# Kernel optimization log

Measured on AMD Instinct MI355X. Metric: run time of the kernel, lower is better.

## Reference

```python
import jax, jax.numpy as jnp
import numpy as np
import math

D_MODEL = 512
NHEAD = 8
HEAD_DIM = D_MODEL // NHEAD
MAX_REL = 128
B, T, S = 4, 2048, 2048


def setup_inputs() -> dict:
    key = jax.random.key(0)
    ks = jax.random.split(key, 16)
    sc = 1.0 / math.sqrt(D_MODEL)
    inp = {
        "query": jax.random.normal(ks[0], (B, T, D_MODEL), jnp.float32),
        "key": jax.random.normal(ks[1], (B, S, D_MODEL), jnp.float32),
        "value": jax.random.normal(ks[2], (B, S, D_MODEL), jnp.float32),
        "Wq": jax.random.normal(ks[3], (D_MODEL, D_MODEL), jnp.float32) * sc,
        "bq": jnp.zeros((D_MODEL,), jnp.float32),
        "Wk": jax.random.normal(ks[4], (D_MODEL, D_MODEL), jnp.float32) * sc,
        "bk": jnp.zeros((D_MODEL,), jnp.float32),
        "Wv": jax.random.normal(ks[5], (D_MODEL, D_MODEL), jnp.float32) * sc,
        "bv": jnp.zeros((D_MODEL,), jnp.float32),
        "Wo": jax.random.normal(ks[6], (D_MODEL, D_MODEL), jnp.float32) * sc,
        "bo": jnp.zeros((D_MODEL,), jnp.float32),
        "rel_emb": jax.random.normal(ks[7], (2 * MAX_REL + 1, NHEAD), jnp.float32) * 0.02,
    }
    return inp


def reference(query, key, value, Wq, bq, Wk, bk, Wv, bv, Wo, bo, rel_emb):
    # linear projections (torch Linear: x @ W.T + b), split heads -> [B,H,T,Dh]
    def proj(x, W, b, L):
        return (x @ W.T + b).reshape(B, L, NHEAD, HEAD_DIM).transpose(0, 2, 1, 3)

    q = proj(query, Wq, bq, T)
    k = proj(key, Wk, bk, S)
    v = proj(value, Wv, bv, S)

    scores = jnp.einsum("bhtd,bhsd->bhts", q, k) / math.sqrt(HEAD_DIM)

    # relative position bias lookup: rel[t,s] = clamp(t-s) + max_rel -> [H,T,S]
    rel = jnp.arange(T)[:, None] - jnp.arange(S)[None, :]
    rel = jnp.clip(rel, -MAX_REL, MAX_REL) + MAX_REL
    bias = rel_emb[rel].transpose(2, 0, 1)  # [H,T,S]
    scores = scores + bias[None]

    w = jax.nn.softmax(scores, axis=-1)  # dropout p used in eval mode -> identity
    out = jnp.einsum("bhts,bhsd->bhtd", w, v)
    out = out.transpose(0, 2, 1, 3).reshape(B, T, D_MODEL)
    return out @ Wo.T + bo
```

## Files before the change

kernel.cpp:

```cpp
#include <hip/hip_runtime.h>

typedef __attribute__((ext_vector_type(4))) float f32x4;
typedef __attribute__((ext_vector_type(16))) float f32x16;
typedef __attribute__((ext_vector_type(4))) unsigned short u16x4;
typedef __attribute__((ext_vector_type(8))) unsigned short u16x8;
typedef __attribute__((ext_vector_type(4))) unsigned int u32x4;
typedef __attribute__((ext_vector_type(8))) __bf16 bf16x8;

#define SZX_E ((size_t)4 * 2048 * 512)
#define SZW_E ((size_t)512 * 512)

__device__ __forceinline__ unsigned short f2bf(float f) {
  unsigned int u = __builtin_bit_cast(unsigned int, f);
  u += 0x7fffu + ((u >> 16) & 1u);
  return (unsigned short)(u >> 16);
}

__device__ __forceinline__ bf16x8 ld_bf8(const unsigned short* p) {
  return __builtin_bit_cast(bf16x8, *(const u16x8*)p);
}

__device__ __forceinline__ f32x4 mfma16(bf16x8 a, bf16x8 b, f32x4 c) {
  return __builtin_amdgcn_mfma_f32_16x16x32_bf16(a, b, c, 0, 0, 0);
}

__device__ __forceinline__ f32x16 mfma32(bf16x8 a, bf16x8 b, f32x16 c) {
  return __builtin_amdgcn_mfma_f32_32x32x16_bf16(a, b, c, 0, 0, 0);
}

__device__ __forceinline__ unsigned int cvt_pk_bf16(float lo, float hi) {
  unsigned int r;
  asm("v_cvt_pk_bf16_f32 %0, %1, %2" : "=v"(r) : "v"(lo), "v"(hi));
  return r;
}

__device__ __forceinline__ void plane32_swap(unsigned int& a, unsigned int& b) {
  asm("v_permlane32_swap_b32 %0, %1" : "+v"(a), "+v"(b));
}

__device__ __forceinline__ float exp2_fast(float x) {
  float r;
  asm("v_exp_f32 %0, %1" : "=v"(r) : "v"(x));
  return r;
}

__device__ __forceinline__ void gload16(const void* g, void* l) {
  __builtin_amdgcn_global_load_lds(
      (const __attribute__((address_space(1))) unsigned int*)g,
      (__attribute__((address_space(3))) unsigned int*)l, 16, 0, 0);
}

__global__ __launch_bounds__(256) void cvt_all(const float* __restrict__ q_,
                                               const float* __restrict__ k_,
                                               const float* __restrict__ v_,
                                               const float* __restrict__ wq_,
                                               const float* __restrict__ wk_,
                                               const float* __restrict__ wv_,
                                               const float* __restrict__ wo_,
                                               unsigned short* __restrict__ out) {
  const int bq = blockIdx.x;
  const float* src;
  size_t segbase, li;
  if (bq < 12288) {
    const int s = bq >> 12;
    src = (s == 0) ? q_ : (s == 1) ? k_ : v_;
    li = (size_t)(bq & 4095) * 256 + threadIdx.x;
    segbase = (size_t)s * 4194304;
  } else {
    const int s = (bq - 12288) >> 8;
    src = (s == 0) ? wq_ : (s == 1) ? wk_ : (s == 2) ? wv_ : wo_;
    li = (size_t)((bq - 12288) & 255) * 256 + threadIdx.x;
    segbase = 12582912 + (size_t)s * 262144;
  }
  const f32x4 v = *(const f32x4*)(src + li * 4);
  u16x4 r;
  r[0] = f2bf(v[0]); r[1] = f2bf(v[1]); r[2] = f2bf(v[2]); r[3] = f2bf(v[3]);
  *(u16x4*)(out + segbase + li * 4) = r;
}

__global__ __launch_bounds__(256) void gemm_qkv(const unsigned short* __restrict__ base,
                                                const float* __restrict__ bq,
                                                const float* __restrict__ bk,
                                                const float* __restrict__ bv,
                                                unsigned short* __restrict__ outb) {
  __shared__ unsigned short Asb[2][4096];
  __shared__ unsigned short Bsb[2][4096];
  const int z = blockIdx.z;
  const unsigned short* A = base + (size_t)z * SZX_E;
  const unsigned short* Bw = base + 3 * SZX_E + (size_t)z * SZW_E;
  const float* bias = (z == 0) ? bq : (z == 1) ? bk : bv;

  const int tid = threadIdx.x;
  const int l = tid & 63;
  const int w = tid >> 6;
  const int g = l >> 4;
  const int lr = l & 15;
  const int mB = blockIdx.y * 128;
  const int nB = blockIdx.x * 128;
  const int m0 = (w >> 1) * 64;
  const int n0 = (w & 1) * 64;
  const int ubase = tid & ~63;

  auto stage = [&](int bufi, int kk) {
#pragma unroll
    for (int i = 0; i < 2; i++) {
      const int idx = i * 256 + tid;
      const int ub = i * 256 + ubase;
      const int r = idx >> 2, c = idx & 3;
      gload16((const char*)A + ((size_t)(mB + r) * 512 + kk + c * 8) * 2,
              (char*)&Asb[bufi][0] + ub * 16);
      gload16((const char*)Bw + ((size_t)(nB + r) * 512 + kk + c * 8) * 2,
              (char*)&Bsb[bufi][0] + ub * 16);
    }
  };

  f32x4 acc[4][4];
#pragma unroll
  for (int i = 0; i < 4; i++)
#pragma unroll
    for (int j = 0; j < 4; j++) acc[i][j] = f32x4{0.f, 0.f, 0.f, 0.f};

  stage(0, 0);
  __syncthreads();
  int buf = 0;

  for (int ks = 0; ks < 16; ++ks) {
    if (ks < 15) stage(buf ^ 1, (ks + 1) * 32);
    bf16x8 af[4], bfr[4];
#pragma unroll
    for (int t = 0; t < 4; t++) {
      af[t] = ld_bf8(&Asb[buf][(m0 + t * 16 + lr) * 32 + g * 8]);
      bfr[t] = ld_bf8(&Bsb[buf][(n0 + t * 16 + lr) * 32 + g * 8]);
    }
#pragma unroll
    for (int i = 0; i < 4; i++)
#pragma unroll
      for (int j = 0; j < 4; j++)
        acc[i][j] = mfma16(af[i], bfr[j], acc[i][j]);
    __syncthreads();
    buf ^= 1;
  }

  unsigned short* outz = outb + (size_t)z * SZX_E;
#pragma unroll
  for (int j = 0; j < 4; j++) {
    const int n = nB + n0 + j * 16 + lr;
    const float bn = bias[n];
#pragma unroll
    for (int i = 0; i < 4; i++) {
#pragma unroll
      for (int r = 0; r < 4; r++) {
        const int m = mB + m0 + i * 16 + g * 4 + r;
        const float v = acc[i][j][r] + bn;
        if (z < 2) {
          outz[(size_t)m * 512 + n] = f2bf(v);
        } else {
          const int bb = m >> 11, s = m & 2047;
          const int hh = n >> 6, d = n & 63;
          outz[((size_t)((bb * 8 + hh) * 64 + d) << 11) + s] = f2bf(v);
        }
      }
    }
  }
}

__global__ __launch_bounds__(256) void gemm_o(const unsigned short* __restrict__ A,
                                              const unsigned short* __restrict__ Bw,
                                              const float* __restrict__ bias,
                                              float* __restrict__ Cout) {
  __shared__ unsigned short Asb[2][4096];
  __shared__ unsigned short Bsb[2][4096];
  const int tid = threadIdx.x;
  const int l = tid & 63;
  const int w = tid >> 6;
  const int g = l >> 4;
  const int lr = l & 15;
  const int mB = blockIdx.y * 128;
  const int nB = blockIdx.x * 128;
  const int m0 = (w >> 1) * 64;
  const int n0 = (w & 1) * 64;
  const int ubase = tid & ~63;

  auto stage = [&](int bufi, int kk) {
#pragma unroll
    for (int i = 0; i < 2; i++) {
      const int idx = i * 256 + tid;
      const int ub = i * 256 + ubase;
      const int r = idx >> 2, c = idx & 3;
      gload16((const char*)A + ((size_t)(mB + r) * 512 + kk + c * 8) * 2,
              (char*)&Asb[bufi][0] + ub * 16);
      gload16((const char*)Bw + ((size_t)(nB + r) * 512 + kk + c * 8) * 2,
              (char*)&Bsb[bufi][0] + ub * 16);
    }
  };

  f32x4 acc[4][4];
#pragma unroll
  for (int i = 0; i < 4; i++)
#pragma unroll
    for (int j = 0; j < 4; j++) acc[i][j] = f32x4{0.f, 0.f, 0.f, 0.f};

  stage(0, 0);
  __syncthreads();
  int buf = 0;

  for (int ks = 0; ks < 16; ++ks) {
    if (ks < 15) stage(buf ^ 1, (ks + 1) * 32);
    bf16x8 af[4], bfr[4];
#pragma unroll
    for (int t = 0; t < 4; t++) {
      af[t] = ld_bf8(&Asb[buf][(m0 + t * 16 + lr) * 32 + g * 8]);
      bfr[t] = ld_bf8(&Bsb[buf][(n0 + t * 16 + lr) * 32 + g * 8]);
    }
#pragma unroll
    for (int i = 0; i < 4; i++)
#pragma unroll
      for (int j = 0; j < 4; j++)
        acc[i][j] = mfma16(af[i], bfr[j], acc[i][j]);
    __syncthreads();
    buf ^= 1;
  }

#pragma unroll
  for (int j = 0; j < 4; j++) {
    const int n = nB + n0 + j * 16 + lr;
    const float bn = bias[n];
#pragma unroll
    for (int i = 0; i < 4; i++) {
#pragma unroll
      for (int r = 0; r < 4; r++) {
        const int m = mB + m0 + i * 16 + g * 4 + r;
        Cout[(size_t)m * 512 + n] = acc[i][j][r] + bn;
      }
    }
  }
}

__global__ __launch_bounds__(256, 2) void attn_kernel(const unsigned short* __restrict__ Qp,
                                                      const unsigned short* __restrict__ Kp,
                                                      const unsigned short* __restrict__ Vt,
                                                      const float* __restrict__ rel_emb,
                                                      unsigned short* __restrict__ At) {
  __shared__ float bias_s[257];
  __shared__ unsigned short K_lds[2][4096];
  __shared__ unsigned short V_lds[2][4096];
  const int bid = blockIdx.x;
  const int qb = bid & 15;
  const int h = (bid >> 4) & 7;
  const int b = bid >> 7;
  const int tid = threadIdx.x;
  const int lane = tid & 63, w = tid >> 6;
  const int hi = lane >> 5, q31 = lane & 31;
  const int q0w = qb * 128 + w * 32;
  const int tq = q0w + q31;
  const float SCL = 0.125f * 1.44269504f;

  const char* kstage = (const char*)Kp + ((size_t)b * 2048 * 512 + h * 64) * 2;
  const char* vstage = (const char*)Vt + ((size_t)(b * 8 + h) * 64 * 2048) * 2;

  auto stage = [&](int bufi, int s0n) {
#pragma unroll
    for (int ii = 0; ii < 4; ii++) {
      const int ins = (w & 1) * 4 + ii;
      const int r = ins * 8 + (lane >> 3);
      const int ch = (lane & 7) ^ (r & 7);
      if (w < 2) {
        gload16(kstage + (size_t)(s0n + r) * 1024 + ch * 16,
                (char*)&K_lds[bufi][0] + ins * 1024);
      } else {
        gload16(vstage + (size_t)r * 4096 + (size_t)s0n * 2 + ch * 16,
                (char*)&V_lds[bufi][0] + ins * 1024);
      }
    }
  };

  for (int i = tid; i < 257; i += 256) bias_s[i] = rel_emb[i * 8 + h] * 1.44269504f;
  stage(0, 0);
  __syncthreads();
  const float bias_lo = bias_s[0], bias_hi = bias_s[256];

  const unsigned short* qptr = Qp + (size_t)(b * 2048 + tq) * 512 + h * 64 + hi * 8;
  const bf16x8 qf0 = ld_bf8(qptr);
  const bf16x8 qf1 = ld_bf8(qptr + 16);
  const bf16x8 qf2 = ld_bf8(qptr + 32);
  const bf16x8 qf3 = ld_bf8(qptr + 48);

  const f32x16 z16 = {0.f, 0.f, 0.f, 0.f, 0.f, 0.f, 0.f, 0.f,
                      0.f, 0.f, 0.f, 0.f, 0.f, 0.f, 0.f, 0.f};
  f32x16 o_lo = z16, o_hi = z16;
  float m_run = -1e30f, l_run = 0.f;
  int buf = 0;

  for (int t = 0; t < 32; ++t) {
    const int s0 = t * 64;
    if (t != 31) stage(buf ^ 1, s0 + 64);

    const unsigned short* kb = &K_lds[buf][0];
    const int rswz = q31 & 7;
    f32x16 sa, sb;
    sa = mfma32(ld_bf8(kb + q31 * 64 + (((0 + hi) ^ rswz) << 3)), qf0, z16);
    sb = mfma32(ld_bf8(kb + (32 + q31) * 64 + (((0 + hi) ^ rswz) << 3)), qf0, z16);
    sa = mfma32(ld_bf8(kb + q31 * 64 + (((2 + hi) ^ rswz) << 3)), qf1, sa);
    sb = mfma32(ld_bf8(kb + (32 + q31) * 64 + (((2 + hi) ^ rswz) << 3)), qf1, sb);
    sa = mfma32(ld_bf8(kb + q31 * 64 + (((4 + hi) ^ rswz) << 3)), qf2, sa);
    sb = mfma32(ld_bf8(kb + (32 + q31) * 64 + (((4 + hi) ^ rswz) << 3)), qf2, sb);
    sa = mfma32(ld_bf8(kb + q31 * 64 + (((6 + hi) ^ rswz) << 3)), qf3, sa);
    sb = mfma32(ld_bf8(kb + (32 + q31) * 64 + (((6 + hi) ^ rswz) << 3)), qf3, sb);

    const unsigned short* vb = &V_lds[buf][0];
    bf16x8 vl[4], vh[4];
#pragma unroll
    for (int ks = 0; ks < 4; ks++) {
      vl[ks] = ld_bf8(vb + q31 * 64 + (((ks * 2 + hi) ^ rswz) << 3));
      vh[ks] = ld_bf8(vb + (32 + q31) * 64 + (((ks * 2 + hi) ^ rswz) << 3));
    }

    const int relmin = q0w - s0 - 63;
    const int relmax = q0w + 31 - s0;
    if (relmin >= 128 || relmax <= -128) {
      const float bc = (relmin >= 128) ? bias_hi : bias_lo;
#pragma unroll
      for (int r = 0; r < 16; r++) {
        sa[r] = fmaf(sa[r], SCL, bc);
        sb[r] = fmaf(sb[r], SCL, bc);
      }
    } else {
#pragma unroll
      for (int r = 0; r < 16; r++) {
        const int rowA = (r & 3) + 8 * (r >> 2) + 4 * hi;
        const int rA = tq - s0 - rowA;
        const int rB = rA - 32;
        const int iA = (rA < -128 ? -128 : (rA > 128 ? 128 : rA)) + 128;
        const int iB = (rB < -128 ? -128 : (rB > 128 ? 128 : rB)) + 128;
        sa[r] = fmaf(sa[r], SCL, bias_s[iA]);
        sb[r] = fmaf(sb[r], SCL, bias_s[iB]);
      }
    }

    const float t0 = fmaxf(fmaxf(sa[0], sa[1]), sa[2]);
    const float t1 = fmaxf(fmaxf(sa[3], sa[4]), sa[5]);
    const float t2 = fmaxf(fmaxf(sa[6], sa[7]), sa[8]);
    const float t3 = fmaxf(fmaxf(sa[9], sa[10]), sa[11]);
    const float t4 = fmaxf(fmaxf(sa[12], sa[13]), sa[14]);
    const float t5 = fmaxf(fmaxf(sa[15], sb[0]), sb[1]);
    const float t6 = fmaxf(fmaxf(sb[2], sb[3]), sb[4]);
    const float t7 = fmaxf(fmaxf(sb[5], sb[6]), sb[7]);
    const float t8 = fmaxf(fmaxf(sb[8], sb[9]), sb[10]);
    const float t9 = fmaxf(fmaxf(sb[11], sb[12]), sb[13]);
    const float ta = fmaxf(sb[14], sb[15]);
    const float u0 = fmaxf(fmaxf(t0, t1), t2);
    const float u1 = fmaxf(fmaxf(t3, t4), t5);
    const float u2 = fmaxf(fmaxf(t6, t7), t8);
    float mx = fmaxf(fmaxf(fmaxf(u0, u1), u2), fmaxf(t9, ta));
    mx = fmaxf(mx, __shfl_xor(mx, 32, 64));

    if (!__all(mx <= m_run + 8.f)) {
      const float m_new = fmaxf(m_run, mx);
      const float rsq = exp2_fast(m_run - m_new);
      l_run *= rsq;
      m_run = m_new;
#pragma unroll
      for (int r2 = 0; r2 < 16; r2++) {
        const int ro = (r2 & 3) + 8 * (r2 >> 2) + 4 * hi;
        const float rr = __shfl(rsq, ro, 64);
        o_lo[r2] *= rr;
        o_hi[r2] *= rr;
      }
    }

#pragma unroll
    for (int r = 0; r < 16; r++) {
      sa[r] = exp2_fast(sa[r] - m_run);
      sb[r] = exp2_fast(sb[r] - m_run);
    }
    float s8[8];
#pragma unroll
    for (int i = 0; i < 8; i++)
      s8[i] = (sa[i] + sa[i + 8]) + (sb[i] + sb[i + 8]);
    float ps = ((s8[0] + s8[1]) + (s8[2] + s8[3])) + ((s8[4] + s8[5]) + (s8[6] + s8[7]));
    ps += __shfl_xor(ps, 32, 64);
    l_run += ps;

    bf16x8 pa[4];
#pragma unroll
    for (int ks = 0; ks < 4; ks++) {
      const int c8 = (ks & 1) * 8;
      const f32x16& src = (ks < 2) ? sa : sb;
      unsigned int a0 = cvt_pk_bf16(src[c8 + 0], src[c8 + 1]);
      unsigned int b0 = cvt_pk_bf16(src[c8 + 4], src[c8 + 5]);
      unsigned int a1 = cvt_pk_bf16(src[c8 + 2], src[c8 + 3]);
      unsigned int b1 = cvt_pk_bf16(src[c8 + 6], src[c8 + 7]);
      plane32_swap(a0, b0);
      plane32_swap(a1, b1);
      pa[ks] = __builtin_bit_cast(bf16x8, u32x4{a0, a1, b0, b1});
    }

#pragma unroll
    for (int ks = 0; ks < 4; ks++) {
      o_lo = mfma32(pa[ks], vl[ks], o_lo);
      o_hi = mfma32(pa[ks], vh[ks], o_hi);
    }

    __syncthreads();
    buf ^= 1;
  }

  const float inv = 1.f / l_run;
#pragma unroll
  for (int r2 = 0; r2 < 16; r2++) {
    const int ro = (r2 & 3) + 8 * (r2 >> 2) + 4 * hi;
    const float rr = __shfl(inv, ro, 64);
    unsigned short* op = At + (size_t)(b * 2048 + q0w + ro) * 512 + h * 64;
    op[q31] = f2bf(o_lo[r2] * rr);
    op[32 + q31] = f2bf(o_hi[r2] * rr);
  }
}

extern "C" void kernel_launch(void* const* d_in, const int* in_sizes, int n_in,
                              void* d_out, int out_size, void* d_ws, size_t ws_size,
                              hipStream_t stream) {
  const float* query = (const float*)d_in[0];
  const float* key   = (const float*)d_in[1];
  const float* value = (const float*)d_in[2];
  const float* Wq = (const float*)d_in[3];
  const float* bq = (const float*)d_in[4];
  const float* Wk = (const float*)d_in[5];
  const float* bk = (const float*)d_in[6];
  const float* Wv = (const float*)d_in[7];
  const float* bv = (const float*)d_in[8];
  const float* Wo = (const float*)d_in[9];
  const float* bo = (const float*)d_in[10];
  const float* rel = (const float*)d_in[11];

  char* ws = (char*)d_ws;
  unsigned short* base = (unsigned short*)ws;
  unsigned short* wo = base + 3 * SZX_E + 3 * SZW_E;
  unsigned short* Qp = base + 3 * SZX_E + 4 * SZW_E;
  unsigned short* Kp = Qp + SZX_E;
  unsigned short* Vt = Kp + SZX_E;
  unsigned short* At = Vt + SZX_E;

  cvt_all<<<dim3(13312), dim3(256), 0, stream>>>(query, key, value, Wq, Wk, Wv, Wo, base);

  dim3 blk(256);
  gemm_qkv<<<dim3(4, 64, 3), blk, 0, stream>>>(base, bq, bk, bv, Qp);

  attn_kernel<<<dim3(512), blk, 0, stream>>>(Qp, Kp, Vt, rel, At);

  gemm_o<<<dim3(4, 64), blk, 0, stream>>>(At, wo, bo, (float*)d_out);
}
```

Measured before the change: 114.0 us.

## Fuse fp32-to-bf16 activation conversion into QKV GEMM staging with padded LDS

Drops the separate pass that converted query/key/value to bf16. The QKV GEMM now loads fp32 rows into registers, converts them, and writes them to LDS itself, which removes a full activation write and re-read. Both GEMMs switch from direct global-to-LDS loads to register-staged loads with a padded row stride of 40 to reduce bank conflicts. The attention kernel also folds the constant-bias scaling into the exp argument for far-off tiles. The trade-off is more VGPR use and loss of async direct-to-LDS copies.

```diff
diff --git a/kernel.cpp b/kernel.cpp
--- a/kernel.cpp
+++ b/kernel.cpp
@@ -9,6 +9,7 @@
 
 #define SZX_E ((size_t)4 * 2048 * 512)
 #define SZW_E ((size_t)512 * 512)
+#define ASTR 40
 
 __device__ __forceinline__ unsigned short f2bf(float f) {
   unsigned int u = __builtin_bit_cast(unsigned int, f);
@@ -50,44 +51,34 @@
       (__attribute__((address_space(3))) unsigned int*)l, 16, 0, 0);
 }
 
-__global__ __launch_bounds__(256) void cvt_all(const float* __restrict__ q_,
-                                               const float* __restrict__ k_,
-                                               const float* __restrict__ v_,
-                                               const float* __restrict__ wq_,
-                                               const float* __restrict__ wk_,
-                                               const float* __restrict__ wv_,
-                                               const float* __restrict__ wo_,
-                                               unsigned short* __restrict__ out) {
+__global__ __launch_bounds__(256) void cvt_w(const float* __restrict__ wq_,
+                                             const float* __restrict__ wk_,
+                                             const float* __restrict__ wv_,
+                                             const float* __restrict__ wo_,
+                                             unsigned short* __restrict__ out) {
   const int bq = blockIdx.x;
-  const float* src;
-  size_t segbase, li;
-  if (bq < 12288) {
-    const int s = bq >> 12;
-    src = (s == 0) ? q_ : (s == 1) ? k_ : v_;
-    li = (size_t)(bq & 4095) * 256 + threadIdx.x;
-    segbase = (size_t)s * 4194304;
-  } else {
-    const int s = (bq - 12288) >> 8;
-    src = (s == 0) ? wq_ : (s == 1) ? wk_ : (s == 2) ? wv_ : wo_;
-    li = (size_t)((bq - 12288) & 255) * 256 + threadIdx.x;
-    segbase = 12582912 + (size_t)s * 262144;
-  }
+  const int s = bq >> 8;
+  const float* src = (s == 0) ? wq_ : (s == 1) ? wk_ : (s == 2) ? wv_ : wo_;
+  const size_t li = (size_t)(bq & 255) * 256 + threadIdx.x;
   const f32x4 v = *(const f32x4*)(src + li * 4);
   u16x4 r;
   r[0] = f2bf(v[0]); r[1] = f2bf(v[1]); r[2] = f2bf(v[2]); r[3] = f2bf(v[3]);
-  *(u16x4*)(out + segbase + li * 4) = r;
-}
-
-__global__ __launch_bounds__(256) void gemm_qkv(const unsigned short* __restrict__ base,
+  *(u16x4*)(out + (size_t)s * SZW_E + li * 4) = r;
+}
+
+__global__ __launch_bounds__(256) void gemm_qkv(const float* __restrict__ q_,
+                                                const float* __restrict__ k_,
+                                                const float* __restrict__ v_,
+                                                const unsigned short* __restrict__ wbase,
                                                 const float* __restrict__ bq,
                                                 const float* __restrict__ bk,
                                                 const float* __restrict__ bv,
                                                 unsigned short* __restrict__ outb) {
-  __shared__ unsigned short Asb[2][4096];
-  __shared__ unsigned short Bsb[2][4096];
+  __shared__ unsigned short Asb[2][128 * ASTR];
+  __shared__ unsigned short Bsb[2][128 * ASTR];
   const int z = blockIdx.z;
-  const unsigned short* A = base + (size_t)z * SZX_E;
-  const unsigned short* Bw = base + 3 * SZX_E + (size_t)z * SZW_E;
+  const float* A = (z == 0) ? q_ : (z == 1) ? k_ : v_;
+  const unsigned short* Bw = wbase + (size_t)z * SZW_E;
   const float* bias = (z == 0) ? bq : (z == 1) ? bk : bv;
 
   const int tid = threadIdx.x;
@@ -99,20 +90,37 @@
   const int nB = blockIdx.x * 128;
   const int m0 = (w >> 1) * 64;
   const int n0 = (w & 1) * 64;
-  const int ubase = tid & ~63;
-
-  auto stage = [&](int bufi, int kk) {
-#pragma unroll
-    for (int i = 0; i < 2; i++) {
-      const int idx = i * 256 + tid;
-      const int ub = i * 256 + ubase;
-      const int r = idx >> 2, c = idx & 3;
-      gload16((const char*)A + ((size_t)(mB + r) * 512 + kk + c * 8) * 2,
-              (char*)&Asb[bufi][0] + ub * 16);
-      gload16((const char*)Bw + ((size_t)(nB + r) * 512 + kk + c * 8) * 2,
-              (char*)&Bsb[bufi][0] + ub * 16);
-    }
+
+  const int r = tid >> 1, h2 = tid & 1;
+  const float* arow = A + (size_t)(mB + r) * 512 + h2 * 16;
+  const unsigned short* brow = Bw + (size_t)(nB + r) * 512 + h2 * 16;
+  const int woff = r * ASTR + h2 * 16;
+
+  f32x4 an[4];
+  u16x8 bn[2];
+  auto loadS = [&](int kk) {
+    an[0] = *(const f32x4*)(arow + kk);
+    an[1] = *(const f32x4*)(arow + kk + 4);
+    an[2] = *(const f32x4*)(arow + kk + 8);
+    an[3] = *(const f32x4*)(arow + kk + 12);
+    bn[0] = *(const u16x8*)(brow + kk);
+    bn[1] = *(const u16x8*)(brow + kk + 8);
   };
+  auto writeS = [&](int bufi) {
+    u32x4 p0, p1;
+    p0[0] = cvt_pk_bf16(an[0][0], an[0][1]);
+    p0[1] = cvt_pk_bf16(an[0][2], an[0][3]);
+    p0[2] = cvt_pk_bf16(an[1][0], an[1][1]);
+    p0[3] = cvt_pk_bf16(an[1][2], an[1][3]);
+    p1[0] = cvt_pk_bf16(an[2][0], an[2][1]);
+    p1[1] = cvt_pk_bf16(an[2][2], an[2][3]);
+    p1[2] = cvt_pk_bf16(an[3][0], an[3][1]);
+    p1[3] = cvt_pk_bf16(an[3][2], an[3][3]);
+    *(u32x4*)(&Asb[bufi][woff]) = p0;
+    *(u32x4*)(&Asb[bufi][woff + 8]) = p1;
+    *(u16x8*)(&Bsb[bufi][woff]) = bn[0];
+    *(u16x8*)(&Bsb[bufi][woff + 8]) = bn[1];
+  };
 
   f32x4 acc[4][4];
 #pragma unroll
@@ -120,23 +128,25 @@
 #pragma unroll
     for (int j = 0; j < 4; j++) acc[i][j] = f32x4{0.f, 0.f, 0.f, 0.f};
 
-  stage(0, 0);
+  loadS(0);
+  writeS(0);
   __syncthreads();
   int buf = 0;
 
   for (int ks = 0; ks < 16; ++ks) {
-    if (ks < 15) stage(buf ^ 1, (ks + 1) * 32);
+    if (ks < 15) loadS((ks + 1) * 32);
     bf16x8 af[4], bfr[4];
 #pragma unroll
     for (int t = 0; t < 4; t++) {
-      af[t] = ld_bf8(&Asb[buf][(m0 + t * 16 + lr) * 32 + g * 8]);
-      bfr[t] = ld_bf8(&Bsb[buf][(n0 + t * 16 + lr) * 32 + g * 8]);
+      af[t] = ld_bf8(&Asb[buf][(m0 + t * 16 + lr) * ASTR + g * 8]);
+      bfr[t] = ld_bf8(&Bsb[buf][(n0 + t * 16 + lr) * ASTR + g * 8]);
     }
 #pragma unroll
     for (int i = 0; i < 4; i++)
 #pragma unroll
       for (int j = 0; j < 4; j++)
         acc[i][j] = mfma16(af[i], bfr[j], acc[i][j]);
+    if (ks < 15) writeS(buf ^ 1);
     __syncthreads();
     buf ^= 1;
   }
@@ -145,13 +155,13 @@
 #pragma unroll
   for (int j = 0; j < 4; j++) {
     const int n = nB + n0 + j * 16 + lr;
-    const float bn = bias[n];
-#pragma unroll
-    for (int i = 0; i < 4; i++) {
-#pragma unroll
-      for (int r = 0; r < 4; r++) {
-        const int m = mB + m0 + i * 16 + g * 4 + r;
-        const float v = acc[i][j][r] + bn;
+    const float bnv = bias[n];
+#pragma unroll
+    for (int rr = 0; rr < 4; rr++) {
+#pragma unroll
+      for (int i = 0; i < 4; i++) {
+        const int m = mB + m0 + i * 16 + g * 4 + rr;
+        const float v = acc[i][j][rr] + bnv;
         if (z < 2) {
           outz[(size_t)m * 512 + n] = f2bf(v);
         } else {
@@ -168,8 +178,8 @@
                                               const unsigned short* __restrict__ Bw,
                                               const float* __restrict__ bias,
                                               float* __restrict__ Cout) {
-  __shared__ unsigned short Asb[2][4096];
-  __shared__ unsigned short Bsb[2][4096];
+  __shared__ unsigned short Asb[2][128 * ASTR];
+  __shared__ unsigned short Bsb[2][128 * ASTR];
   const int tid = threadIdx.x;
   const int l = tid & 63;
   const int w = tid >> 6;
@@ -179,20 +189,25 @@
   const int nB = blockIdx.x * 128;
   const int m0 = (w >> 1) * 64;
   const int n0 = (w & 1) * 64;
-  const int ubase = tid & ~63;
-
-  auto stage = [&](int bufi, int kk) {
-#pragma unroll
-    for (int i = 0; i < 2; i++) {
-      const int idx = i * 256 + tid;
-      const int ub = i * 256 + ubase;
-      const int r = idx >> 2, c = idx & 3;
-      gload16((const char*)A + ((size_t)(mB + r) * 512 + kk + c * 8) * 2,
-              (char*)&Asb[bufi][0] + ub * 16);
-      gload16((const char*)Bw + ((size_t)(nB + r) * 512 + kk + c * 8) * 2,
-              (char*)&Bsb[bufi][0] + ub * 16);
-    }
+
+  const int r = tid >> 1, h2 = tid & 1;
+  const unsigned short* arow = A + (size_t)(mB + r) * 512 + h2 * 16;
+  const unsigned short* brow = Bw + (size_t)(nB + r) * 512 + h2 * 16;
+  const int woff = r * ASTR + h2 * 16;
+
+  u16x8 an[2], bn[2];
+  auto loadS = [&](int kk) {
+    an[0] = *(const u16x8*)(arow + kk);
+    an[1] = *(const u16x8*)(arow + kk + 8);
+    bn[0] = *(const u16x8*)(brow + kk);
+    bn[1] = *(const u16x8*)(brow + kk + 8);
   };
+  auto writeS = [&](int bufi) {
+    *(u16x8*)(&Asb[bufi][woff]) = an[0];
+    *(u16x8*)(&Asb[bufi][woff + 8]) = an[1];
+    *(u16x8*)(&Bsb[bufi][woff]) = bn[0];
+    *(u16x8*)(&Bsb[bufi][woff + 8]) = bn[1];
+  };
 
   f32x4 acc[4][4];
 #pragma unroll
@@ -200,23 +215,25 @@
 #pragma unroll
     for (int j = 0; j < 4; j++) acc[i][j] = f32x4{0.f, 0.f, 0.f, 0.f};
 
-  stage(0, 0);
+  loadS(0);
+  writeS(0);
   __syncthreads();
   int buf = 0;
 
   for (int ks = 0; ks < 16; ++ks) {
-    if (ks < 15) stage(buf ^ 1, (ks + 1) * 32);
+    if (ks < 15) loadS((ks + 1) * 32);
     bf16x8 af[4], bfr[4];
 #pragma unroll
     for (int t = 0; t < 4; t++) {
-      af[t] = ld_bf8(&Asb[buf][(m0 + t * 16 + lr) * 32 + g * 8]);
-      bfr[t] = ld_bf8(&Bsb[buf][(n0 + t * 16 + lr) * 32 + g * 8]);
+      af[t] = ld_bf8(&Asb[buf][(m0 + t * 16 + lr) * ASTR + g * 8]);
+      bfr[t] = ld_bf8(&Bsb[buf][(n0 + t * 16 + lr) * ASTR + g * 8]);
     }
 #pragma unroll
     for (int i = 0; i < 4; i++)
 #pragma unroll
       for (int j = 0; j < 4; j++)
         acc[i][j] = mfma16(af[i], bfr[j], acc[i][j]);
+    if (ks < 15) writeS(buf ^ 1);
     __syncthreads();
     buf ^= 1;
   }
@@ -224,13 +241,13 @@
 #pragma unroll
   for (int j = 0; j < 4; j++) {
     const int n = nB + n0 + j * 16 + lr;
-    const float bn = bias[n];
-#pragma unroll
-    for (int i = 0; i < 4; i++) {
-#pragma unroll
-      for (int r = 0; r < 4; r++) {
-        const int m = mB + m0 + i * 16 + g * 4 + r;
-        Cout[(size_t)m * 512 + n] = acc[i][j][r] + bn;
+    const float bnv = bias[n];
+#pragma unroll
+    for (int rr = 0; rr < 4; rr++) {
+#pragma unroll
+      for (int i = 0; i < 4; i++) {
+        const int m = mB + m0 + i * 16 + g * 4 + rr;
+        Cout[(size_t)m * 512 + n] = acc[i][j][rr] + bnv;
       }
     }
   }
@@ -262,13 +279,13 @@
 #pragma unroll
     for (int ii = 0; ii < 4; ii++) {
       const int ins = (w & 1) * 4 + ii;
-      const int r = ins * 8 + (lane >> 3);
-      const int ch = (lane & 7) ^ (r & 7);
+      const int rr = ins * 8 + (lane >> 3);
+      const int ch = (lane & 7) ^ (rr & 7);
       if (w < 2) {
-        gload16(kstage + (size_t)(s0n + r) * 1024 + ch * 16,
+        gload16(kstage + (size_t)(s0n + rr) * 1024 + ch * 16,
                 (char*)&K_lds[bufi][0] + ins * 1024);
       } else {
-        gload16(vstage + (size_t)r * 4096 + (size_t)s0n * 2 + ch * 16,
+        gload16(vstage + (size_t)rr * 4096 + (size_t)s0n * 2 + ch * 16,
                 (char*)&V_lds[bufi][0] + ins * 1024);
       }
     }
@@ -317,13 +334,10 @@
 
     const int relmin = q0w - s0 - 63;
     const int relmax = q0w + 31 - s0;
+    float SCL2, off0;
     if (relmin >= 128 || relmax <= -128) {
-      const float bc = (relmin >= 128) ? bias_hi : bias_lo;
-#pragma unroll
-      for (int r = 0; r < 16; r++) {
-        sa[r] = fmaf(sa[r], SCL, bc);
-        sb[r] = fmaf(sb[r], SCL, bc);
-      }
+      SCL2 = SCL;
+      off0 = (relmin >= 128) ? bias_hi : bias_lo;
     } else {
 #pragma unroll
       for (int r = 0; r < 16; r++) {
@@ -335,6 +349,8 @@
         sa[r] = fmaf(sa[r], SCL, bias_s[iA]);
         sb[r] = fmaf(sb[r], SCL, bias_s[iB]);
       }
+      SCL2 = 1.f;
+      off0 = 0.f;
     }
 
     const float t0 = fmaxf(fmaxf(sa[0], sa[1]), sa[2]);
@@ -352,6 +368,7 @@
     const float u1 = fmaxf(fmaxf(t3, t4), t5);
     const float u2 = fmaxf(fmaxf(t6, t7), t8);
     float mx = fmaxf(fmaxf(fmaxf(u0, u1), u2), fmaxf(t9, ta));
+    mx = fmaf(mx, SCL2, off0);
     mx = fmaxf(mx, __shfl_xor(mx, 32, 64));
 
     if (!__all(mx <= m_run + 8.f)) {
@@ -368,10 +385,11 @@
       }
     }
 
+    const float ea = off0 - m_run;
 #pragma unroll
     for (int r = 0; r < 16; r++) {
-      sa[r] = exp2_fast(sa[r] - m_run);
-      sb[r] = exp2_fast(sb[r] - m_run);
+      sa[r] = exp2_fast(fmaf(sa[r], SCL2, ea));
+      sb[r] = exp2_fast(fmaf(sb[r], SCL2, ea));
     }
     float s8[8];
 #pragma unroll
@@ -433,19 +451,18 @@
   const float* rel = (const float*)d_in[11];
 
   char* ws = (char*)d_ws;
-  unsigned short* base = (unsigned short*)ws;
-  unsigned short* wo = base + 3 * SZX_E + 3 * SZW_E;
-  unsigned short* Qp = base + 3 * SZX_E + 4 * SZW_E;
+  unsigned short* wgt = (unsigned short*)ws;
+  unsigned short* Qp = wgt + 4 * SZW_E;
   unsigned short* Kp = Qp + SZX_E;
   unsigned short* Vt = Kp + SZX_E;
   unsigned short* At = Vt + SZX_E;
 
-  cvt_all<<<dim3(13312), dim3(256), 0, stream>>>(query, key, value, Wq, Wk, Wv, Wo, base);
-
   dim3 blk(256);
-  gemm_qkv<<<dim3(4, 64, 3), blk, 0, stream>>>(base, bq, bk, bv, Qp);
+  cvt_w<<<dim3(1024), blk, 0, stream>>>(Wq, Wk, Wv, Wo, wgt);
+
+  gemm_qkv<<<dim3(4, 64, 3), blk, 0, stream>>>(query, key, value, wgt, bq, bk, bv, Qp);
 
   attn_kernel<<<dim3(512), blk, 0, stream>>>(Qp, Kp, Vt, rel, At);
 
-  gemm_o<<<dim3(4, 64), blk, 0, stream>>>(At, wo, bo, (float*)d_out);
-}
+  gemm_o<<<dim3(4, 64), blk, 0, stream>>>(At, wgt + 3 * SZW_E, bo, (float*)d_out);
+}
```

After: 115.6 us. No clear change (+1.4%).
